# Performance work log

Measured on AMD Instinct MI355X. Metric: run time of the kernel, lower is better.

Reference implementation:

```python
import jax, jax.numpy as jnp
import numpy as np

N = 50000
NEG_SLOPE = 0.2


def gat_conv(x, src, dst, W, a_src, a_dst, bias, heads, out_ch, concat):
    n = x.shape[0]
    h = (x @ W).reshape(n, heads, out_ch)            # [N, H, C]
    alpha_s = jnp.einsum('nhc,hc->nh', h, a_src)      # [N, H]
    alpha_d = jnp.einsum('nhc,hc->nh', h, a_dst)
    e = alpha_s[src] + alpha_d[dst]                   # [E, H]
    e = jax.nn.leaky_relu(e, NEG_SLOPE)
    # segment softmax over destination node (PyG: softmax over index=dst)
    m = jax.ops.segment_max(e, dst, num_segments=n)
    e = jnp.exp(e - m[dst])
    s = jax.ops.segment_sum(e, dst, num_segments=n)
    alpha = e / (s[dst] + 1e-16)                      # [E, H]
    msg = h[src] * alpha[:, :, None]                  # [E, H, C]
    out = jax.ops.segment_sum(msg, dst, num_segments=n)  # [N, H, C]
    out = out.reshape(n, heads * out_ch) if concat else out.mean(axis=1)
    return out + bias


def setup_inputs() -> dict:
    key = jax.random.key(0)
    ks = jax.random.split(key, 12)
    F_in, H, C1, NC = 512, 8, 16, 64
    E = 800000
    x = jax.random.normal(ks[0], (N, F_in), dtype=jnp.float32)
    edge_index = jax.random.randint(ks[1], (2, E), 0, N, dtype=jnp.int64)
    def glorot(k, shape):
        fan = shape[0] + shape[-1]
        lim = jnp.sqrt(6.0 / fan).astype(jnp.float32)
        return jax.random.uniform(k, shape, jnp.float32, -lim, lim)
    W1 = glorot(ks[2], (F_in, H * C1))
    att_src1 = glorot(ks[3], (H, C1))
    att_dst1 = glorot(ks[4], (H, C1))
    b1 = jnp.zeros((H * C1,), jnp.float32)
    W2 = glorot(ks[5], (H * C1, NC))
    att_src2 = glorot(ks[6], (1, NC))
    att_dst2 = glorot(ks[7], (1, NC))
    b2 = jnp.zeros((NC,), jnp.float32)
    return {"x": x, "edge_index": edge_index,
            "W1": W1, "att_src1": att_src1, "att_dst1": att_dst1, "b1": b1,
            "W2": W2, "att_src2": att_src2, "att_dst2": att_dst2, "b2": b2}


def reference(x, edge_index, W1, att_src1, att_dst1, b1, W2, att_src2, att_dst2, b2):
    # PyG GATConv default add_self_loops=True
    loops = jnp.arange(N, dtype=edge_index.dtype)
    src = jnp.concatenate([edge_index[0], loops])
    dst = jnp.concatenate([edge_index[1], loops])
    h = gat_conv(x, src, dst, W1, att_src1, att_dst1, b1, heads=8, out_ch=16, concat=True)
    h = jax.nn.relu(h)
    out = gat_conv(h, src, dst, W2, att_src2, att_dst2, b2, heads=1, out_ch=64, concat=False)
    return jax.nn.log_softmax(out, axis=1)
```

## Files before the change

### kernel.cpp

```cpp
#include <hip/hip_runtime.h>
#include <math.h>

#define N_NODES 50000
#define FIN 512
#define H1 8
#define D1 128
#define D2 64
#define NSCB ((N_NODES + 1023) >> 10)
#define GG 1563

typedef __attribute__((ext_vector_type(4))) float f32x4;
typedef __attribute__((ext_vector_type(8))) __bf16 bf16x8;
typedef __attribute__((ext_vector_type(4))) __bf16 bf16x4;

__device__ __forceinline__ void gload_lds16(const void* g, void* l) {
    __builtin_amdgcn_global_load_lds(
        (const __attribute__((address_space(1))) void*)g,
        (__attribute__((address_space(3))) void*)l, 16, 0, 0);
}

__global__ __launch_bounds__(256) void k_prep(const float* __restrict__ W1,
                                              const float* __restrict__ W2,
                                              __bf16* __restrict__ WpP,
                                              __bf16* __restrict__ Wp2,
                                              int* __restrict__ cnt) {
    int idx = blockIdx.x * 256 + threadIdx.x;
    int k = idx >> 7, col = idx & 127;
    int region = k >> 6;
    int kgl = (k >> 3) & 7;
    int u_out = (kgl * 128 + col) ^ (kgl & 3);
    WpP[region * 8192 + u_out * 8 + (k & 7)] = (__bf16)W1[idx];
    if (idx < N_NODES) cnt[idx] = 0;
    if (idx < D1 * D2) {
        int k2 = idx >> 6, col2 = idx & 63;
        Wp2[(k2 >> 3) * 512 + col2 * 8 + (k2 & 7)] = (__bf16)W2[idx];
    }
}

__global__ __launch_bounds__(256) void k_mega(const float* __restrict__ x,
                                              const __bf16* __restrict__ WpP,
                                              const float* __restrict__ asrc1,
                                              const float* __restrict__ adst1,
                                              __bf16* __restrict__ h1b,
                                              float* __restrict__ as1,
                                              float* __restrict__ ad1,
                                              const int* __restrict__ ei, int E,
                                              int* __restrict__ cnt,
                                              int* __restrict__ rank) {
    __shared__ __align__(16) __bf16 As[32 * 64];
    __shared__ __align__(16) __bf16 Bs[64 * 128];
    const int t = threadIdx.x;

    if (blockIdx.x >= GG) {
        int e = (blockIdx.x - GG) * 256 + t;
        int ET = E + N_NODES;
        if (e < ET) {
            int d = (e < E) ? ei[E + e] : (e - E);
            rank[e] = atomicAdd(&cnt[d], 1);
        }
        return;
    }

    const int l = t & 63;
    const int w = t >> 6;
    const int wr = (w >> 1) * 16, wc = (w & 1) * 64;
    const int n0 = blockIdx.x * 32;

    f32x4 acc[4];
    #pragma unroll
    for (int j = 0; j < 4; ++j) acc[j] = (f32x4){0.f, 0.f, 0.f, 0.f};

    const int arow = t >> 4;
    const int ak4  = (t & 15) * 4;

    for (int s = 0; s < 8; ++s) {
        const int k0 = s * 64;
        {
            const __bf16* gsrc = WpP + (size_t)s * 8192;
            #pragma unroll
            for (int i = 0; i < 4; ++i) {
                int ubase = w * 256 + i * 64;
                gload_lds16(gsrc + (ubase + l) * 8, Bs + ubase * 8);
            }
        }
        #pragma unroll
        for (int i = 0; i < 2; ++i) {
            int row = arow + i * 16;
            int grow = n0 + row;
            float4 f = {0.f, 0.f, 0.f, 0.f};
            if (grow < N_NODES)
                f = *(const float4*)(x + (size_t)grow * FIN + k0 + ak4);
            bf16x4 v = {(__bf16)f.x, (__bf16)f.y, (__bf16)f.z, (__bf16)f.w};
            int eo = (row * 64 + ak4) ^ ((row & 7) << 3);
            *(bf16x4*)(As + eo) = v;
        }
        __syncthreads();
        #pragma unroll
        for (int ks = 0; ks < 2; ++ks) {
            bf16x8 af, bfr[4];
            {
                int row = wr + (l & 15);
                int eo = (row * 64 + ks * 32 + (l >> 4) * 8) ^ ((row & 7) << 3);
                af = *(const bf16x8*)(As + eo);
            }
            #pragma unroll
            for (int fn = 0; fn < 4; ++fn) {
                int col = wc + fn * 16 + (l & 15);
                int kg = ks * 4 + (l >> 4);
                int u = (kg * 128 + col) ^ (kg & 3);
                bfr[fn] = *(const bf16x8*)(Bs + u * 8);
            }
            #pragma unroll
            for (int fn = 0; fn < 4; ++fn)
                acc[fn] = __builtin_amdgcn_mfma_f32_16x16x32_bf16(
                    af, bfr[fn], acc[fn], 0, 0, 0);
        }
        __syncthreads();
    }
    #pragma unroll
    for (int reg = 0; reg < 4; ++reg) {
        int row = n0 + wr + (l >> 4) * 4 + reg;
        if (row >= N_NODES) continue;
        #pragma unroll
        for (int fn = 0; fn < 4; ++fn) {
            int col = wc + fn * 16 + (l & 15);
            h1b[(size_t)row * D1 + col] = (__bf16)acc[fn][reg];
        }
    }
    const int c16 = l & 15;
    float av[4], dv[4];
    #pragma unroll
    for (int fn = 0; fn < 4; ++fn) {
        int head = (wc >> 4) + fn;
        av[fn] = asrc1[head * 16 + c16];
        dv[fn] = adst1[head * 16 + c16];
    }
    #pragma unroll
    for (int reg = 0; reg < 4; ++reg) {
        #pragma unroll
        for (int fn = 0; fn < 4; ++fn) {
            float vs = acc[fn][reg] * av[fn];
            float vd = acc[fn][reg] * dv[fn];
            #pragma unroll
            for (int mk = 1; mk <= 8; mk <<= 1) {
                vs += __shfl_xor(vs, mk, 64);
                vd += __shfl_xor(vd, mk, 64);
            }
            if (c16 == 0) {
                int row = n0 + wr + (l >> 4) * 4 + reg;
                if (row < N_NODES) {
                    int head = (wc >> 4) + fn;
                    as1[(size_t)row * 8 + head] = vs;
                    ad1[(size_t)row * 8 + head] = vd;
                }
            }
        }
    }
}

__global__ __launch_bounds__(256) void k_scan1(const int* __restrict__ cnt,
                                               int* __restrict__ basep,
                                               int* __restrict__ aux) {
    __shared__ int lds[256];
    int t = threadIdx.x, b = blockIdx.x;
    int g = b * 1024 + t * 4;
    int v0 = (g + 0 < N_NODES) ? cnt[g + 0] : 0;
    int v1 = (g + 1 < N_NODES) ? cnt[g + 1] : 0;
    int v2 = (g + 2 < N_NODES) ? cnt[g + 2] : 0;
    int v3 = (g + 3 < N_NODES) ? cnt[g + 3] : 0;
    int tsum = v0 + v1 + v2 + v3;
    lds[t] = tsum; __syncthreads();
    for (int off = 1; off < 256; off <<= 1) {
        int add = (t >= off) ? lds[t - off] : 0;
        __syncthreads();
        lds[t] += add;
        __syncthreads();
    }
    int excl = lds[t] - tsum;
    if (g + 0 < N_NODES) basep[g + 0] = excl;
    if (g + 1 < N_NODES) basep[g + 1] = excl + v0;
    if (g + 2 < N_NODES) basep[g + 2] = excl + v0 + v1;
    if (g + 3 < N_NODES) basep[g + 3] = excl + v0 + v1 + v2;
    if (t == 255) aux[b] = lds[255];
}

__global__ __launch_bounds__(64) void k_scan2(const int* __restrict__ aux,
                                              int* __restrict__ auxs) {
    int t = threadIdx.x;
    int v = (t < NSCB) ? aux[t] : 0;
    int orig = v;
    for (int off = 1; off < 64; off <<= 1) {
        int x = __shfl_up(v, off, 64);
        if (t >= off) v += x;
    }
    auxs[t] = v - orig;
}

__global__ __launch_bounds__(256) void k_scatter(const int* __restrict__ ei, int E,
                                                 const int* __restrict__ basep,
                                                 const int* __restrict__ auxs,
                                                 const int* __restrict__ rank,
                                                 int* __restrict__ srcs) {
    int e = blockIdx.x * 256 + threadIdx.x;
    int ET = E + N_NODES;
    if (e >= ET) return;
    int s = (e < E) ? ei[e] : (e - E);
    int d = (e < E) ? ei[E + e] : (e - E);
    int pos = basep[d] + auxs[d >> 10] + rank[e];
    __builtin_nontemporal_store(s, &srcs[pos]);
}

__global__ __launch_bounds__(256) void k_agg1(const int* __restrict__ basep,
                                              const int* __restrict__ auxs,
                                              const int* __restrict__ srcs,
                                              const float* __restrict__ as1,
                                              const float* __restrict__ ad1,
                                              const __bf16* __restrict__ h1b,
                                              const float* __restrict__ b1,
                                              __bf16* __restrict__ r1b, int ET) {
    __shared__ float elds[4][512];
    const int w = threadIdx.x >> 6;
    const int l = threadIdx.x & 63;
    const int q = l >> 4;
    const int c8 = (l & 15) * 8;
    const int h = (l & 15) >> 1;
    const int n = blockIdx.x * 4 + w;
    const int p0 = basep[n] + auxs[n >> 10];
    const int p1 = (n + 1 < N_NODES) ? basep[n + 1] + auxs[(n + 1) >> 10] : ET;
    const int m = p1 - p0;
    float adv[8];
    #pragma unroll
    for (int i = 0; i < 8; ++i) adv[i] = ad1[(size_t)n * 8 + i];
    float ac[8] = {0.f, 0.f, 0.f, 0.f, 0.f, 0.f, 0.f, 0.f};
    float se = 0.f;
    for (int base = 0; base < m; base += 64) {
        const int cm = min(64, m - base);
        asm volatile("s_waitcnt lgkmcnt(0)" ::: "memory");
        int my_s = 0;
        if (l < cm) {
            my_s = srcs[p0 + base + l];
            const float4* ap = (const float4*)(as1 + (size_t)my_s * 8);
            float4 A0 = ap[0], A1 = ap[1];
            float uu[8] = {A0.x + adv[0], A0.y + adv[1], A0.z + adv[2], A0.w + adv[3],
                           A1.x + adv[4], A1.y + adv[5], A1.z + adv[6], A1.w + adv[7]};
            float ee[8];
            #pragma unroll
            for (int i = 0; i < 8; ++i) {
                float u = uu[i];
                u = (u > 0.f) ? u : 0.2f * u;
                ee[i] = __expf(u);
            }
            *(float4*)(&elds[w][l * 8])     = make_float4(ee[0], ee[1], ee[2], ee[3]);
            *(float4*)(&elds[w][l * 8 + 4]) = make_float4(ee[4], ee[5], ee[6], ee[7]);
        }
        asm volatile("s_waitcnt lgkmcnt(0)" ::: "memory");
        #pragma unroll 2
        for (int j4 = 0; j4 < cm; j4 += 4) {
            int j = j4 + q;
            bool ok = j < cm;
            int jj = ok ? j : 0;
            int s = __shfl(my_s, jj, 64);
            float ee = elds[w][jj * 8 + h];
            if (!ok) ee = 0.f;
            se += ee;
            bf16x8 hv = *(const bf16x8*)(h1b + (size_t)s * D1 + c8);
            #pragma unroll
            for (int i = 0; i < 8; ++i) ac[i] += ee * (float)hv[i];
        }
    }
    #pragma unroll
    for (int mk = 16; mk <= 32; mk <<= 1) {
        #pragma unroll
        for (int i = 0; i < 8; ++i) ac[i] += __shfl_xor(ac[i], mk, 64);
        se += __shfl_xor(se, mk, 64);
    }
    if (q == 0) {
        float inv = 1.f / (se + 1e-16f);
        bf16x8 r;
        #pragma unroll
        for (int i = 0; i < 8; ++i)
            r[i] = (__bf16)fmaxf(ac[i] * inv + b1[c8 + i], 0.f);
        *(bf16x8*)(r1b + (size_t)n * D1 + c8) = r;
    }
}

__global__ __launch_bounds__(256) void k_gemm2(const __bf16* __restrict__ r1b,
                                               const __bf16* __restrict__ Wp2,
                                               const float* __restrict__ av2,
                                               const float* __restrict__ dv2,
                                               __bf16* __restrict__ h2b,
                                               float* __restrict__ as2,
                                               float* __restrict__ ad2) {
    __shared__ __align__(16) __bf16 As[128 * 128];
    __shared__ __align__(16) __bf16 Bs[128 * 64];
    const int t = threadIdx.x;
    const int l = t & 63;
    const int w = t >> 6;
    const int wr = w * 32;
    const int n0 = blockIdx.x * 128;

    const uint4* gb = (const uint4*)Wp2;
    #pragma unroll
    for (int i = 0; i < 4; ++i) {
        int u = t + i * 256;
        uint4 d = gb[u];
        int u2 = u ^ ((u >> 6) & 3);
        *(uint4*)(Bs + u2 * 8) = d;
    }
    #pragma unroll
    for (int i = 0; i < 8; ++i) {
        int u = t + i * 256;
        int row = u >> 4, koff = (u & 15) * 8;
        bf16x8 v = {};
        if (n0 + row < N_NODES)
            v = *(const bf16x8*)(r1b + (size_t)(n0 + row) * D1 + koff);
        int eo = (row * 128 + koff) ^ ((row & 7) << 3);
        *(bf16x8*)(As + eo) = v;
    }
    __syncthreads();

    f32x4 acc[2][4];
    #pragma unroll
    for (int i = 0; i < 2; ++i)
        #pragma unroll
        for (int j = 0; j < 4; ++j) acc[i][j] = (f32x4){0.f, 0.f, 0.f, 0.f};

    #pragma unroll
    for (int ks = 0; ks < 4; ++ks) {
        bf16x8 af[2], bfr[4];
        #pragma unroll
        for (int fm = 0; fm < 2; ++fm) {
            int row = wr + fm * 16 + (l & 15);
            int eo = (row * 128 + ks * 32 + (l >> 4) * 8) ^ ((row & 7) << 3);
            af[fm] = *(const bf16x8*)(As + eo);
        }
        #pragma unroll
        for (int fn = 0; fn < 4; ++fn) {
            int col = fn * 16 + (l & 15);
            int kg = ks * 4 + (l >> 4);
            int u = (kg * 64 + col) ^ (kg & 3);
            bfr[fn] = *(const bf16x8*)(Bs + u * 8);
        }
        #pragma unroll
        for (int fm = 0; fm < 2; ++fm)
            #pragma unroll
            for (int fn = 0; fn < 4; ++fn)
                acc[fm][fn] = __builtin_amdgcn_mfma_f32_16x16x32_bf16(
                    af[fm], bfr[fn], acc[fm][fn], 0, 0, 0);
    }
    #pragma unroll
    for (int fm = 0; fm < 2; ++fm) {
        #pragma unroll
        for (int reg = 0; reg < 4; ++reg) {
            int row = n0 + wr + fm * 16 + (l >> 4) * 4 + reg;
            if (row >= N_NODES) continue;
            #pragma unroll
            for (int fn = 0; fn < 4; ++fn) {
                int col = fn * 16 + (l & 15);
                h2b[(size_t)row * D2 + col] = (__bf16)acc[fm][fn][reg];
            }
        }
    }
    const int c16 = l & 15;
    float av[4], dv[4];
    #pragma unroll
    for (int fn = 0; fn < 4; ++fn) {
        av[fn] = av2[fn * 16 + c16];
        dv[fn] = dv2[fn * 16 + c16];
    }
    #pragma unroll
    for (int fm = 0; fm < 2; ++fm) {
        #pragma unroll
        for (int reg = 0; reg < 4; ++reg) {
            float vs = 0.f, vd = 0.f;
            #pragma unroll
            for (int fn = 0; fn < 4; ++fn) {
                vs += acc[fm][fn][reg] * av[fn];
                vd += acc[fm][fn][reg] * dv[fn];
            }
            #pragma unroll
            for (int mk = 1; mk <= 8; mk <<= 1) {
                vs += __shfl_xor(vs, mk, 64);
                vd += __shfl_xor(vd, mk, 64);
            }
            if (c16 == 0) {
                int row = n0 + wr + fm * 16 + (l >> 4) * 4 + reg;
                if (row < N_NODES) { as2[row] = vs; ad2[row] = vd; }
            }
        }
    }
}

__global__ __launch_bounds__(256) void k_agg2(const int* __restrict__ basep,
                                              const int* __restrict__ auxs,
                                              const int* __restrict__ srcs,
                                              const float* __restrict__ as2,
                                              const float* __restrict__ ad2,
                                              const __bf16* __restrict__ h2b,
                                              const float* __restrict__ b2,
                                              float* __restrict__ out, int ET) {
    const int w = threadIdx.x >> 6;
    const int l = threadIdx.x & 63;
    const int o = l >> 3;
    const int c8 = (l & 7) * 8;
    const int n = blockIdx.x * 4 + w;
    const int p0 = basep[n] + auxs[n >> 10];
    const int p1 = (n + 1 < N_NODES) ? basep[n + 1] + auxs[(n + 1) >> 10] : ET;
    const int m = p1 - p0;
    const float adn = ad2[n];
    float ac[8] = {0.f, 0.f, 0.f, 0.f, 0.f, 0.f, 0.f, 0.f};
    float se = 0.f;
    for (int base = 0; base < m; base += 64) {
        const int cm = min(64, m - base);
        int my_s = 0; float my_e = 0.f;
        if (l < cm) {
            my_s = srcs[p0 + base + l];
            float u = as2[my_s] + adn;
            u = (u > 0.f) ? u : 0.2f * u;
            my_e = __expf(u);
        }
        #pragma unroll 2
        for (int j8 = 0; j8 < cm; j8 += 8) {
            int j = j8 + o;
            bool ok = j < cm;
            int jj = ok ? j : 0;
            int s = __shfl(my_s, jj, 64);
            float ee = __shfl(my_e, jj, 64);
            if (!ok) ee = 0.f;
            se += ee;
            bf16x8 hv = *(const bf16x8*)(h2b + (size_t)s * D2 + c8);
            #pragma unroll
            for (int i = 0; i < 8; ++i) ac[i] += ee * (float)hv[i];
        }
    }
    #pragma unroll
    for (int mk = 8; mk <= 32; mk <<= 1) {
        #pragma unroll
        for (int i = 0; i < 8; ++i) ac[i] += __shfl_xor(ac[i], mk, 64);
        se += __shfl_xor(se, mk, 64);
    }
    float inv = 1.f / (se + 1e-16f);
    float v[8];
    #pragma unroll
    for (int i = 0; i < 8; ++i) v[i] = ac[i] * inv + b2[c8 + i];
    float mx = v[0];
    #pragma unroll
    for (int i = 1; i < 8; ++i) mx = fmaxf(mx, v[i]);
    #pragma unroll
    for (int mk = 1; mk <= 4; mk <<= 1) mx = fmaxf(mx, __shfl_xor(mx, mk, 64));
    float ex = 0.f;
    #pragma unroll
    for (int i = 0; i < 8; ++i) ex += __expf(v[i] - mx);
    #pragma unroll
    for (int mk = 1; mk <= 4; mk <<= 1) ex += __shfl_xor(ex, mk, 64);
    float lse = mx + __logf(ex);
    if (o == 0) {
        f32x4 r0 = {v[0] - lse, v[1] - lse, v[2] - lse, v[3] - lse};
        f32x4 r1 = {v[4] - lse, v[5] - lse, v[6] - lse, v[7] - lse};
        *(f32x4*)(out + (size_t)n * D2 + c8)     = r0;
        *(f32x4*)(out + (size_t)n * D2 + c8 + 4) = r1;
    }
}

extern "C" void kernel_launch(void* const* d_in, const int* in_sizes, int n_in,
                              void* d_out, int out_size, void* d_ws, size_t ws_size,
                              hipStream_t stream) {
    const float* x     = (const float*)d_in[0];
    const int*   ei    = (const int*)d_in[1];
    const float* W1    = (const float*)d_in[2];
    const float* asrc1 = (const float*)d_in[3];
    const float* adst1 = (const float*)d_in[4];
    const float* b1    = (const float*)d_in[5];
    const float* W2    = (const float*)d_in[6];
    const float* asrc2 = (const float*)d_in[7];
    const float* adst2 = (const float*)d_in[8];
    const float* b2    = (const float*)d_in[9];

    const int E  = in_sizes[1] / 2;
    const int ET = E + N_NODES;

    __bf16* r1b = (__bf16*)d_ws;
    float* fw  = (float*)(r1b + (size_t)N_NODES * D1);
    float* as1  = fw;
    float* ad1  = as1  + (size_t)N_NODES * H1;
    float* as2  = ad1  + (size_t)N_NODES * H1;
    float* ad2  = as2  + N_NODES;
    int* iw   = (int*)(ad2 + N_NODES);
    int* cnt  = iw;
    int* basep= cnt  + N_NODES;
    int* aux  = basep + N_NODES + 1;
    int* auxs = aux  + 64;
    int* rank = auxs + 64;
    int* srcs = rank + ET;
    uintptr_t pa = ((uintptr_t)(srcs + ET) + 255) & ~(uintptr_t)255;
    __bf16* WpP  = (__bf16*)pa;
    __bf16* Wp2  = WpP + (size_t)FIN * D1;
    __bf16* h1b  = Wp2 + (size_t)D1 * D2;
    __bf16* h2b  = h1b + (size_t)N_NODES * D1;

    const int gE = (ET + 255) / 256;

    k_prep   <<<FIN * D1 / 256, 256, 0, stream>>>(W1, W2, WpP, Wp2, cnt);
    k_mega   <<<GG + gE, 256, 0, stream>>>(x, WpP, asrc1, adst1, h1b, as1, ad1,
                                           ei, E, cnt, rank);
    k_scan1  <<<NSCB, 256, 0, stream>>>(cnt, basep, aux);
    k_scan2  <<<1, 64, 0, stream>>>(aux, auxs);
    k_scatter<<<gE, 256, 0, stream>>>(ei, E, basep, auxs, rank, srcs);

    k_agg1   <<<N_NODES / 4, 256, 0, stream>>>(basep, auxs, srcs, as1, ad1, h1b, b1, r1b, ET);
    k_gemm2  <<<(N_NODES + 127) / 128, 256, 0, stream>>>(r1b, Wp2, asrc2, adst2, h2b, as2, ad2);
    k_agg2   <<<N_NODES / 4, 256, 0, stream>>>(basep, auxs, srcs, as2, ad2, h2b, b2, (float*)d_out, ET);
}
```

Baseline: 161.2 us.

## Drop LDS staging in layer-1 GEMM, load MFMA operands directly from global

The first-layer GEMM no longer stages x and W1 tiles through shared memory with async global-to-LDS loads and two barriers per k-step. Each lane now reads its A fragment straight from x in fp32, converts it to bf16, and reads B fragments from a simpler packed W1 layout in global memory, relying on L1/L2 cache for reuse. This removes LDS traffic and barriers. In exchange, W1 is fetched redundantly by every wave and the x loads are less coalesced, since each lane reads 32 bytes from a different row.

```diff
diff --git a/kernel.cpp b/kernel.cpp
--- a/kernel.cpp
+++ b/kernel.cpp
@@ -13,23 +13,14 @@
 typedef __attribute__((ext_vector_type(8))) __bf16 bf16x8;
 typedef __attribute__((ext_vector_type(4))) __bf16 bf16x4;
 
-__device__ __forceinline__ void gload_lds16(const void* g, void* l) {
-    __builtin_amdgcn_global_load_lds(
-        (const __attribute__((address_space(1))) void*)g,
-        (__attribute__((address_space(3))) void*)l, 16, 0, 0);
-}
-
 __global__ __launch_bounds__(256) void k_prep(const float* __restrict__ W1,
                                               const float* __restrict__ W2,
-                                              __bf16* __restrict__ WpP,
+                                              __bf16* __restrict__ Wp,
                                               __bf16* __restrict__ Wp2,
                                               int* __restrict__ cnt) {
     int idx = blockIdx.x * 256 + threadIdx.x;
     int k = idx >> 7, col = idx & 127;
-    int region = k >> 6;
-    int kgl = (k >> 3) & 7;
-    int u_out = (kgl * 128 + col) ^ (kgl & 3);
-    WpP[region * 8192 + u_out * 8 + (k & 7)] = (__bf16)W1[idx];
+    Wp[(k >> 3) * 1024 + col * 8 + (k & 7)] = (__bf16)W1[idx];
     if (idx < N_NODES) cnt[idx] = 0;
     if (idx < D1 * D2) {
         int k2 = idx >> 6, col2 = idx & 63;
@@ -38,7 +29,7 @@
 }
 
 __global__ __launch_bounds__(256) void k_mega(const float* __restrict__ x,
-                                              const __bf16* __restrict__ WpP,
+                                              const __bf16* __restrict__ Wp,
                                               const float* __restrict__ asrc1,
                                               const float* __restrict__ adst1,
                                               __bf16* __restrict__ h1b,
@@ -47,8 +38,6 @@
                                               const int* __restrict__ ei, int E,
                                               int* __restrict__ cnt,
                                               int* __restrict__ rank) {
-    __shared__ __align__(16) __bf16 As[32 * 64];
-    __shared__ __align__(16) __bf16 Bs[64 * 128];
     const int t = threadIdx.x;
 
     if (blockIdx.x >= GG) {
@@ -65,69 +54,48 @@
     const int w = t >> 6;
     const int wr = (w >> 1) * 16, wc = (w & 1) * 64;
     const int n0 = blockIdx.x * 32;
+    const int kg = l >> 4;
+    const int c16 = l & 15;
+
+    const int row = n0 + wr + c16;
+    const bool rowok = row < N_NODES;
+    const float* xrow = x + (size_t)(rowok ? row : 0) * FIN + kg * 8;
 
     f32x4 acc[4];
     #pragma unroll
     for (int j = 0; j < 4; ++j) acc[j] = (f32x4){0.f, 0.f, 0.f, 0.f};
 
-    const int arow = t >> 4;
-    const int ak4  = (t & 15) * 4;
-
-    for (int s = 0; s < 8; ++s) {
-        const int k0 = s * 64;
-        {
-            const __bf16* gsrc = WpP + (size_t)s * 8192;
-            #pragma unroll
-            for (int i = 0; i < 4; ++i) {
-                int ubase = w * 256 + i * 64;
-                gload_lds16(gsrc + (ubase + l) * 8, Bs + ubase * 8);
-            }
-        }
-        #pragma unroll
-        for (int i = 0; i < 2; ++i) {
-            int row = arow + i * 16;
-            int grow = n0 + row;
-            float4 f = {0.f, 0.f, 0.f, 0.f};
-            if (grow < N_NODES)
-                f = *(const float4*)(x + (size_t)grow * FIN + k0 + ak4);
-            bf16x4 v = {(__bf16)f.x, (__bf16)f.y, (__bf16)f.z, (__bf16)f.w};
-            int eo = (row * 64 + ak4) ^ ((row & 7) << 3);
-            *(bf16x4*)(As + eo) = v;
-        }
-        __syncthreads();
-        #pragma unroll
-        for (int ks = 0; ks < 2; ++ks) {
-            bf16x8 af, bfr[4];
-            {
-                int row = wr + (l & 15);
-                int eo = (row * 64 + ks * 32 + (l >> 4) * 8) ^ ((row & 7) << 3);
-                af = *(const bf16x8*)(As + eo);
-            }
-            #pragma unroll
-            for (int fn = 0; fn < 4; ++fn) {
-                int col = wc + fn * 16 + (l & 15);
-                int kg = ks * 4 + (l >> 4);
-                int u = (kg * 128 + col) ^ (kg & 3);
-                bfr[fn] = *(const bf16x8*)(Bs + u * 8);
-            }
-            #pragma unroll
-            for (int fn = 0; fn < 4; ++fn)
-                acc[fn] = __builtin_amdgcn_mfma_f32_16x16x32_bf16(
-                    af, bfr[fn], acc[fn], 0, 0, 0);
-        }
-        __syncthreads();
+    const __bf16* wbase = Wp + (size_t)(wc + c16) * 8 + (size_t)kg * 1024;
+
+    #pragma unroll 2
+    for (int ks = 0; ks < 16; ++ks) {
+        float4 a0 = {0.f, 0.f, 0.f, 0.f}, a1 = {0.f, 0.f, 0.f, 0.f};
+        if (rowok) {
+            a0 = *(const float4*)(xrow + ks * 32);
+            a1 = *(const float4*)(xrow + ks * 32 + 4);
+        }
+        bf16x8 af = {(__bf16)a0.x, (__bf16)a0.y, (__bf16)a0.z, (__bf16)a0.w,
+                     (__bf16)a1.x, (__bf16)a1.y, (__bf16)a1.z, (__bf16)a1.w};
+        const __bf16* wk = wbase + (size_t)ks * 4096;
+        bf16x8 bfr[4];
+        #pragma unroll
+        for (int fn = 0; fn < 4; ++fn)
+            bfr[fn] = *(const bf16x8*)(wk + fn * 128);
+        #pragma unroll
+        for (int fn = 0; fn < 4; ++fn)
+            acc[fn] = __builtin_amdgcn_mfma_f32_16x16x32_bf16(
+                af, bfr[fn], acc[fn], 0, 0, 0);
     }
     #pragma unroll
     for (int reg = 0; reg < 4; ++reg) {
-        int row = n0 + wr + (l >> 4) * 4 + reg;
-        if (row >= N_NODES) continue;
+        int orow = n0 + wr + kg * 4 + reg;
+        if (orow >= N_NODES) continue;
         #pragma unroll
         for (int fn = 0; fn < 4; ++fn) {
-            int col = wc + fn * 16 + (l & 15);
-            h1b[(size_t)row * D1 + col] = (__bf16)acc[fn][reg];
-        }
-    }
-    const int c16 = l & 15;
+            int col = wc + fn * 16 + c16;
+            h1b[(size_t)orow * D1 + col] = (__bf16)acc[fn][reg];
+        }
+    }
     float av[4], dv[4];
     #pragma unroll
     for (int fn = 0; fn < 4; ++fn) {
@@ -147,11 +115,11 @@
                 vd += __shfl_xor(vd, mk, 64);
             }
             if (c16 == 0) {
-                int row = n0 + wr + (l >> 4) * 4 + reg;
-                if (row < N_NODES) {
+                int orow = n0 + wr + kg * 4 + reg;
+                if (orow < N_NODES) {
                     int head = (wc >> 4) + fn;
-                    as1[(size_t)row * 8 + head] = vs;
-                    ad1[(size_t)row * 8 + head] = vd;
+                    as1[(size_t)orow * 8 + head] = vs;
+                    ad1[(size_t)orow * 8 + head] = vd;
                 }
             }
         }
@@ -493,15 +461,15 @@
     int* rank = auxs + 64;
     int* srcs = rank + ET;
     uintptr_t pa = ((uintptr_t)(srcs + ET) + 255) & ~(uintptr_t)255;
-    __bf16* WpP  = (__bf16*)pa;
-    __bf16* Wp2  = WpP + (size_t)FIN * D1;
+    __bf16* Wp   = (__bf16*)pa;
+    __bf16* Wp2  = Wp  + (size_t)FIN * D1;
     __bf16* h1b  = Wp2 + (size_t)D1 * D2;
     __bf16* h2b  = h1b + (size_t)N_NODES * D1;
 
     const int gE = (ET + 255) / 256;
 
-    k_prep   <<<FIN * D1 / 256, 256, 0, stream>>>(W1, W2, WpP, Wp2, cnt);
-    k_mega   <<<GG + gE, 256, 0, stream>>>(x, WpP, asrc1, adst1, h1b, as1, ad1,
+    k_prep   <<<FIN * D1 / 256, 256, 0, stream>>>(W1, W2, Wp, Wp2, cnt);
+    k_mega   <<<GG + gE, 256, 0, stream>>>(x, Wp, asrc1, adst1, h1b, as1, ad1,
                                            ei, E, cnt, rank);
     k_scan1  <<<NSCB, 256, 0, stream>>>(cnt, basep, aux);
     k_scan2  <<<1, 64, 0, stream>>>(aux, auxs);
```

After: 181.8 us. 12.8% more time.

## Fuse layer-2 linear projection into layer-1 aggregation kernel

Applied to the files above, without the earlier changes.

Removes the separate MFMA GEMM2 kernel and the bf16 r1b intermediate. Each wavefront now writes its node's ReLU'd layer-1 output to LDS and computes the 64-wide W2 projection in fp32 with a transposed W2 held in global memory, then the attention dot products via shuffles. This saves a launch and the write and re-read of the N×128 intermediate. In exchange it uses scalar FMAs instead of tensor cores and adds 128 W2 loads per lane per node.

```diff
diff --git a/kernel.cpp b/kernel.cpp
--- a/kernel.cpp
+++ b/kernel.cpp
@@ -22,7 +22,7 @@
 __global__ __launch_bounds__(256) void k_prep(const float* __restrict__ W1,
                                               const float* __restrict__ W2,
                                               __bf16* __restrict__ WpP,
-                                              __bf16* __restrict__ Wp2,
+                                              float* __restrict__ W2T,
                                               int* __restrict__ cnt) {
     int idx = blockIdx.x * 256 + threadIdx.x;
     int k = idx >> 7, col = idx & 127;
@@ -32,8 +32,8 @@
     WpP[region * 8192 + u_out * 8 + (k & 7)] = (__bf16)W1[idx];
     if (idx < N_NODES) cnt[idx] = 0;
     if (idx < D1 * D2) {
-        int k2 = idx >> 6, col2 = idx & 63;
-        Wp2[(k2 >> 3) * 512 + col2 * 8 + (k2 & 7)] = (__bf16)W2[idx];
+        int k2 = idx >> 6, c2 = idx & 63;
+        W2T[c2 * D1 + k2] = W2[idx];
     }
 }
 
@@ -217,7 +217,12 @@
                                               const float* __restrict__ ad1,
                                               const __bf16* __restrict__ h1b,
                                               const float* __restrict__ b1,
-                                              __bf16* __restrict__ r1b, int ET) {
+                                              const float* __restrict__ W2T,
+                                              const float* __restrict__ av2,
+                                              const float* __restrict__ dv2,
+                                              __bf16* __restrict__ h2b,
+                                              float* __restrict__ as2,
+                                              float* __restrict__ ad2, int ET) {
     __shared__ float elds[4][512];
     const int w = threadIdx.x >> 6;
     const int l = threadIdx.x & 63;
@@ -274,121 +279,31 @@
         for (int i = 0; i < 8; ++i) ac[i] += __shfl_xor(ac[i], mk, 64);
         se += __shfl_xor(se, mk, 64);
     }
+    asm volatile("s_waitcnt lgkmcnt(0)" ::: "memory");
     if (q == 0) {
         float inv = 1.f / (se + 1e-16f);
-        bf16x8 r;
         #pragma unroll
         for (int i = 0; i < 8; ++i)
-            r[i] = (__bf16)fmaxf(ac[i] * inv + b1[c8 + i], 0.f);
-        *(bf16x8*)(r1b + (size_t)n * D1 + c8) = r;
-    }
-}
-
-__global__ __launch_bounds__(256) void k_gemm2(const __bf16* __restrict__ r1b,
-                                               const __bf16* __restrict__ Wp2,
-                                               const float* __restrict__ av2,
-                                               const float* __restrict__ dv2,
-                                               __bf16* __restrict__ h2b,
-                                               float* __restrict__ as2,
-                                               float* __restrict__ ad2) {
-    __shared__ __align__(16) __bf16 As[128 * 128];
-    __shared__ __align__(16) __bf16 Bs[128 * 64];
-    const int t = threadIdx.x;
-    const int l = t & 63;
-    const int w = t >> 6;
-    const int wr = w * 32;
-    const int n0 = blockIdx.x * 128;
-
-    const uint4* gb = (const uint4*)Wp2;
-    #pragma unroll
-    for (int i = 0; i < 4; ++i) {
-        int u = t + i * 256;
-        uint4 d = gb[u];
-        int u2 = u ^ ((u >> 6) & 3);
-        *(uint4*)(Bs + u2 * 8) = d;
-    }
-    #pragma unroll
-    for (int i = 0; i < 8; ++i) {
-        int u = t + i * 256;
-        int row = u >> 4, koff = (u & 15) * 8;
-        bf16x8 v = {};
-        if (n0 + row < N_NODES)
-            v = *(const bf16x8*)(r1b + (size_t)(n0 + row) * D1 + koff);
-        int eo = (row * 128 + koff) ^ ((row & 7) << 3);
-        *(bf16x8*)(As + eo) = v;
-    }
-    __syncthreads();
-
-    f32x4 acc[2][4];
-    #pragma unroll
-    for (int i = 0; i < 2; ++i)
-        #pragma unroll
-        for (int j = 0; j < 4; ++j) acc[i][j] = (f32x4){0.f, 0.f, 0.f, 0.f};
-
-    #pragma unroll
-    for (int ks = 0; ks < 4; ++ks) {
-        bf16x8 af[2], bfr[4];
-        #pragma unroll
-        for (int fm = 0; fm < 2; ++fm) {
-            int row = wr + fm * 16 + (l & 15);
-            int eo = (row * 128 + ks * 32 + (l >> 4) * 8) ^ ((row & 7) << 3);
-            af[fm] = *(const bf16x8*)(As + eo);
-        }
-        #pragma unroll
-        for (int fn = 0; fn < 4; ++fn) {
-            int col = fn * 16 + (l & 15);
-            int kg = ks * 4 + (l >> 4);
-            int u = (kg * 64 + col) ^ (kg & 3);
-            bfr[fn] = *(const bf16x8*)(Bs + u * 8);
-        }
-        #pragma unroll
-        for (int fm = 0; fm < 2; ++fm)
-            #pragma unroll
-            for (int fn = 0; fn < 4; ++fn)
-                acc[fm][fn] = __builtin_amdgcn_mfma_f32_16x16x32_bf16(
-                    af[fm], bfr[fn], acc[fm][fn], 0, 0, 0);
-    }
-    #pragma unroll
-    for (int fm = 0; fm < 2; ++fm) {
-        #pragma unroll
-        for (int reg = 0; reg < 4; ++reg) {
-            int row = n0 + wr + fm * 16 + (l >> 4) * 4 + reg;
-            if (row >= N_NODES) continue;
-            #pragma unroll
-            for (int fn = 0; fn < 4; ++fn) {
-                int col = fn * 16 + (l & 15);
-                h2b[(size_t)row * D2 + col] = (__bf16)acc[fm][fn][reg];
-            }
-        }
-    }
-    const int c16 = l & 15;
-    float av[4], dv[4];
-    #pragma unroll
-    for (int fn = 0; fn < 4; ++fn) {
-        av[fn] = av2[fn * 16 + c16];
-        dv[fn] = dv2[fn * 16 + c16];
-    }
-    #pragma unroll
-    for (int fm = 0; fm < 2; ++fm) {
-        #pragma unroll
-        for (int reg = 0; reg < 4; ++reg) {
-            float vs = 0.f, vd = 0.f;
-            #pragma unroll
-            for (int fn = 0; fn < 4; ++fn) {
-                vs += acc[fm][fn][reg] * av[fn];
-                vd += acc[fm][fn][reg] * dv[fn];
-            }
-            #pragma unroll
-            for (int mk = 1; mk <= 8; mk <<= 1) {
-                vs += __shfl_xor(vs, mk, 64);
-                vd += __shfl_xor(vd, mk, 64);
-            }
-            if (c16 == 0) {
-                int row = n0 + wr + fm * 16 + (l >> 4) * 4 + reg;
-                if (row < N_NODES) { as2[row] = vs; ad2[row] = vd; }
-            }
-        }
-    }
+            elds[w][c8 + i] = fmaxf(ac[i] * inv + b1[c8 + i], 0.f);
+    }
+    asm volatile("s_waitcnt lgkmcnt(0)" ::: "memory");
+    const float4* wt = (const float4*)(W2T + (size_t)l * D1);
+    float h2c = 0.f;
+    #pragma unroll 4
+    for (int k4 = 0; k4 < D1 / 4; ++k4) {
+        float4 r4 = *(const float4*)(&elds[w][k4 * 4]);
+        float4 w4 = wt[k4];
+        h2c += r4.x * w4.x + r4.y * w4.y + r4.z * w4.z + r4.w * w4.w;
+    }
+    h2b[(size_t)n * D2 + l] = (__bf16)h2c;
+    float vs = h2c * av2[l];
+    float vd = h2c * dv2[l];
+    #pragma unroll
+    for (int mk = 1; mk <= 32; mk <<= 1) {
+        vs += __shfl_xor(vs, mk, 64);
+        vd += __shfl_xor(vd, mk, 64);
+    }
+    if (l == 0) { as2[n] = vs; ad2[n] = vd; }
 }
 
 __global__ __launch_bounds__(256) void k_agg2(const int* __restrict__ basep,
@@ -479,13 +394,13 @@
     const int E  = in_sizes[1] / 2;
     const int ET = E + N_NODES;
 
-    __bf16* r1b = (__bf16*)d_ws;
-    float* fw  = (float*)(r1b + (size_t)N_NODES * D1);
+    float* fw  = (float*)d_ws;
     float* as1  = fw;
     float* ad1  = as1  + (size_t)N_NODES * H1;
     float* as2  = ad1  + (size_t)N_NODES * H1;
     float* ad2  = as2  + N_NODES;
-    int* iw   = (int*)(ad2 + N_NODES);
+    float* W2T  = ad2  + N_NODES;
+    int* iw   = (int*)(W2T + D1 * D2);
     int* cnt  = iw;
     int* basep= cnt  + N_NODES;
     int* aux  = basep + N_NODES + 1;
@@ -494,20 +409,20 @@
     int* srcs = rank + ET;
     uintptr_t pa = ((uintptr_t)(srcs + ET) + 255) & ~(uintptr_t)255;
     __bf16* WpP  = (__bf16*)pa;
-    __bf16* Wp2  = WpP + (size_t)FIN * D1;
-    __bf16* h1b  = Wp2 + (size_t)D1 * D2;
+    __bf16* h1b  = WpP + (size_t)FIN * D1;
     __bf16* h2b  = h1b + (size_t)N_NODES * D1;
 
     const int gE = (ET + 255) / 256;
 
-    k_prep   <<<FIN * D1 / 256, 256, 0, stream>>>(W1, W2, WpP, Wp2, cnt);
+    k_prep   <<<FIN * D1 / 256, 256, 0, stream>>>(W1, W2, WpP, W2T, cnt);
     k_mega   <<<GG + gE, 256, 0, stream>>>(x, WpP, asrc1, adst1, h1b, as1, ad1,
                                            ei, E, cnt, rank);
     k_scan1  <<<NSCB, 256, 0, stream>>>(cnt, basep, aux);
     k_scan2  <<<1, 64, 0, stream>>>(aux, auxs);
     k_scatter<<<gE, 256, 0, stream>>>(ei, E, basep, auxs, rank, srcs);
 
-    k_agg1   <<<N_NODES / 4, 256, 0, stream>>>(basep, auxs, srcs, as1, ad1, h1b, b1, r1b, ET);
-    k_gemm2  <<<(N_NODES + 127) / 128, 256, 0, stream>>>(r1b, Wp2, asrc2, adst2, h2b, as2, ad2);
-    k_agg2   <<<N_NODES / 4, 256, 0, stream>>>(basep, auxs, srcs, as2, ad2, h2b, b2, (float*)d_out, ET);
-}
+    k_agg1   <<<N_NODES / 4, 256, 0, stream>>>(basep, auxs, srcs, as1, ad1, h1b, b1,
+                                               W2T, asrc2, adst2, h2b, as2, ad2, ET);
+    k_agg2   <<<N_NODES / 4, 256, 0, stream>>>(basep, auxs, srcs, as2, ad2, h2b, b2,
+                                               (float*)d_out, ET);
+}
```

Result: slower. 319.8 us (+98.4%).
